# Kernel tuning notes

Hardware: AMD Instinct MI355X
Metric: run time of the kernel (lower is better)

## Reference

```python
import jax, jax.numpy as jnp
import numpy as np

NUM_HEADS = 16
HEAD_SIZE = 64
EMB = NUM_HEADS * HEAD_SIZE
B, S = 2, 2048


def setup_inputs() -> dict:
    key = jax.random.key(0)
    ks = jax.random.split(key, 8)
    return {
        "values": jax.random.normal(ks[0], (B, S, EMB), dtype=jnp.float32),
        "keys": jax.random.normal(ks[1], (B, S, EMB), dtype=jnp.float32),
        "queries": jax.random.normal(ks[2], (B, S, EMB), dtype=jnp.float32),
        "mask": jnp.ones((B, 1, 1, S), dtype=jnp.int32),
        "Wq": jax.random.normal(ks[3], (HEAD_SIZE, HEAD_SIZE), dtype=jnp.float32) / np.sqrt(HEAD_SIZE),
        "Wk": jax.random.normal(ks[4], (HEAD_SIZE, HEAD_SIZE), dtype=jnp.float32) / np.sqrt(HEAD_SIZE),
        "Wv": jax.random.normal(ks[5], (HEAD_SIZE, HEAD_SIZE), dtype=jnp.float32) / np.sqrt(HEAD_SIZE),
        "Wout": jax.random.normal(ks[6], (EMB, EMB), dtype=jnp.float32) / np.sqrt(EMB),
        "bout": jax.random.normal(ks[7], (EMB,), dtype=jnp.float32) * 0.01,
    }


def reference(values, keys, queries, mask, Wq, Wk, Wv, Wout, bout):
    n, q_len, E = queries.shape
    H, D = NUM_HEADS, HEAD_SIZE
    # split heads: [n, len, H, D]
    v = values.reshape(n, -1, H, D)
    k = keys.reshape(n, -1, H, D)
    q = queries.reshape(n, q_len, H, D)
    # per-head shared linears (torch Linear: x @ W.T), no bias
    v = jnp.einsum("nkhd,cd->nkhc", v, Wv)
    k = jnp.einsum("nkhd,cd->nkhc", k, Wk)
    q = jnp.einsum("nqhd,cd->nqhc", q, Wq)
    # scores: [n, H, q, k]
    energy = jnp.einsum("nqhd,nkhd->nhqk", q, k)
    energy = jnp.where(mask == 0, jnp.float32(-1e28), energy)
    # NOTE: source scales by sqrt(embedding_size), not head_size
    attn = jax.nn.softmax(energy / jnp.sqrt(jnp.float32(E)), axis=3)
    out = jnp.einsum("nhqk,nkhd->nqhd", attn, v).reshape(n, q_len, E)
    return out @ Wout.T + bout
```

## Files before the change

kernel.cpp:

```cpp
#include <hip/hip_runtime.h>
#include <hip/hip_bf16.h>


#define NHB 16
#define HS  64
#define EMB 1024
#define BB  2
#define SS  2048
#define NT  (SS / 64)

typedef __bf16 bf16_t;
typedef bf16_t bf16x8 __attribute__((ext_vector_type(8)));
typedef bf16_t bf16x4 __attribute__((ext_vector_type(4)));
typedef float  f32x4  __attribute__((ext_vector_type(4)));

__device__ __forceinline__ f32x4 mfma16(bf16x8 a, bf16x8 b, f32x4 c) {
    return __builtin_amdgcn_mfma_f32_16x16x32_bf16(a, b, c, 0, 0, 0);
}

__global__ __launch_bounds__(512) void proj_kernel(
    const float* __restrict__ queries, const float* __restrict__ keys,
    const float* __restrict__ values,
    const float* __restrict__ Wq, const float* __restrict__ Wk,
    const float* __restrict__ Wv,
    bf16_t* __restrict__ Qb, bf16_t* __restrict__ Kb, bf16_t* __restrict__ Vt)
{
    __shared__ bf16_t Ws[3][64][72];
    __shared__ bf16_t Xs[128][72];

    const int tid  = threadIdx.x;
    const int wave = tid >> 6, lane = tid & 63;
    const int q4 = lane >> 4, l16 = lane & 15;
    const int s0 = blockIdx.x * 128;
    const int h  = blockIdx.y, n = blockIdx.z;

    #pragma unroll
    for (int i = 0; i < 6; ++i) {
        int g = i * 512 + tid;
        int mW = g >> 10;
        int idx4 = g & 1023;
        const float* wp = (mW == 0) ? Wq : (mW == 1) ? Wk : Wv;
        float4 v = ((const float4*)wp)[idx4];
        int r = idx4 >> 4, c = (idx4 & 15) * 4;
        Ws[mW][r][c+0] = (bf16_t)v.x; Ws[mW][r][c+1] = (bf16_t)v.y;
        Ws[mW][r][c+2] = (bf16_t)v.z; Ws[mW][r][c+3] = (bf16_t)v.w;
    }

    const size_t headBase = (size_t)(n * NHB + h) * SS * HS;

    float4 gx[4];
    auto loadX = [&](const float* xp) {
        #pragma unroll
        for (int i = 0; i < 4; ++i) {
            int idx4 = i * 512 + tid;
            int r = idx4 >> 4, c = (idx4 & 15) * 4;
            gx[i] = *(const float4*)&xp[((size_t)(n * SS + s0 + r)) * EMB + h * HS + c];
        }
    };
    loadX(queries);

    for (int p = 0; p < 3; ++p) {
        __syncthreads();
        #pragma unroll
        for (int i = 0; i < 4; ++i) {
            int idx4 = i * 512 + tid;
            int r = idx4 >> 4, c = (idx4 & 15) * 4;
            Xs[r][c+0] = (bf16_t)gx[i].x; Xs[r][c+1] = (bf16_t)gx[i].y;
            Xs[r][c+2] = (bf16_t)gx[i].z; Xs[r][c+3] = (bf16_t)gx[i].w;
        }
        if (p == 0) loadX(keys);
        else if (p == 1) loadX(values);
        __syncthreads();

        bf16x8 xf[2], wf[4][2];
        #pragma unroll
        for (int kk = 0; kk < 2; ++kk)
            xf[kk] = *(const bf16x8*)&Xs[wave * 16 + l16][kk * 32 + q4 * 8];
        #pragma unroll
        for (int ct = 0; ct < 4; ++ct)
            #pragma unroll
            for (int kk = 0; kk < 2; ++kk)
                wf[ct][kk] = *(const bf16x8*)&Ws[p][ct * 16 + l16][kk * 32 + q4 * 8];

        if (p < 2) {
            bf16_t* dst = (p == 0) ? Qb : Kb;
            const float sc = (p == 0) ? 0.03125f : 1.0f;
            #pragma unroll
            for (int ct = 0; ct < 4; ++ct) {
                f32x4 acc = {};
                acc = mfma16(wf[ct][0], xf[0], acc);
                acc = mfma16(wf[ct][1], xf[1], acc);
                bf16x4 pk;
                #pragma unroll
                for (int i = 0; i < 4; ++i) pk[i] = (bf16_t)(acc[i] * sc);
                *(bf16x4*)&dst[headBase + (size_t)(s0 + wave * 16 + l16) * HS
                               + ct * 16 + q4 * 4] = pk;
            }
        } else {
            #pragma unroll
            for (int ct = 0; ct < 4; ++ct) {
                f32x4 acc = {};
                acc = mfma16(xf[0], wf[ct][0], acc);
                acc = mfma16(xf[1], wf[ct][1], acc);
                bf16x4 pk;
                #pragma unroll
                for (int i = 0; i < 4; ++i) pk[i] = (bf16_t)acc[i];
                *(bf16x4*)&Vt[headBase + (size_t)(ct * 16 + l16) * SS
                              + s0 + (wave >> 1) * 32 + q4 * 8 + (wave & 1) * 4] = pk;
            }
        }
    }
}

__global__ __launch_bounds__(512) void attn_kernel(
    const bf16_t* __restrict__ Qb, const bf16_t* __restrict__ Kb,
    const bf16_t* __restrict__ Vt, const int* __restrict__ mask,
    bf16_t* __restrict__ Og)
{
    __shared__ __align__(16) unsigned char smem[37376];
    auto Ks = (bf16_t(*)[64][72])(smem);
    auto Vs = (bf16_t(*)[64][72])(smem + 18432);
    auto Ms = (float(*)[64])(smem + 36864);
    float* fbuf = (float*)smem;
    float* lbuf = (float*)(smem + 32768);

    const int tid = threadIdx.x;
    const int w = tid >> 6, lane = tid & 63;
    const int q4 = lane >> 4, l16 = lane & 15;
    const int wq = w & 3, wk = w >> 2;
    const int qt = blockIdx.x, h = blockIdx.y, n = blockIdx.z;
    const size_t headBase = (size_t)(n * NHB + h) * SS * HS;
    const int* mrow = mask + n * SS;

    const int sr = tid >> 3, sc = (tid & 7) * 8;
    const bf16_t* kb_src = Kb + headBase + (size_t)sr * HS + sc;
    const bf16_t* vt_src = Vt + headBase + (size_t)sr * SS + sc;

    bf16x8 bq[2][2];
    #pragma unroll
    for (int st = 0; st < 2; ++st) {
        const bf16_t* qptr = Qb + headBase
            + (size_t)(qt * 128 + wq * 32 + st * 16 + l16) * HS;
        bq[st][0] = *(const bf16x8*)&qptr[q4 * 8];
        bq[st][1] = *(const bf16x8*)&qptr[32 + q4 * 8];
    }

    bf16x8 ones;
    #pragma unroll
    for (int i = 0; i < 8; ++i) ones[i] = (bf16_t)1.0f;

    f32x4 oaccT[2][4] = {};
    f32x4 lacc[2] = {};

    *(bf16x8*)&Ks[0][sr][sc] = *(const bf16x8*)kb_src;
    *(bf16x8*)&Vs[0][sr][sc] = *(const bf16x8*)vt_src;
    if (tid < 64) Ms[0][tid] = mrow[tid] ? 0.0f : -3e38f;
    __syncthreads();

    for (int kt = 0; kt < NT; ++kt) {
        const int cur = kt & 1;
        const bool has_next = (kt + 1) < NT;
        bf16x8 gk, gv; float gm = 0.f;
        if (has_next) {
            const int k0n = (kt + 1) * 64;
            gk = *(const bf16x8*)(kb_src + (size_t)k0n * HS);
            gv = *(const bf16x8*)(vt_src + k0n);
            if (tid < 64) gm = mrow[k0n + tid] ? 0.0f : -3e38f;
        }

        f32x4 sacc[2][2];
        #pragma unroll
        for (int c2 = 0; c2 < 2; ++c2) {
            const int ct = wk * 2 + c2;
            float4 bias = *(const float4*)&Ms[cur][ct * 16 + q4 * 4];
            f32x4 b4 = {bias.x, bias.y, bias.z, bias.w};
            sacc[0][c2] = b4; sacc[1][c2] = b4;
            bf16x8 ak0 = *(const bf16x8*)&Ks[cur][ct * 16 + l16][q4 * 8];
            bf16x8 ak1 = *(const bf16x8*)&Ks[cur][ct * 16 + l16][32 + q4 * 8];
            #pragma unroll
            for (int st = 0; st < 2; ++st) {
                sacc[st][c2] = mfma16(ak0, bq[st][0], sacc[st][c2]);
                sacc[st][c2] = mfma16(ak1, bq[st][1], sacc[st][c2]);
            }
        }

        bf16x4 pv[2][2];
        #pragma unroll
        for (int c2 = 0; c2 < 2; ++c2)
            #pragma unroll
            for (int st = 0; st < 2; ++st) {
                bf16x4 pk;
                #pragma unroll
                for (int j = 0; j < 4; ++j)
                    pk[j] = (bf16_t)__expf(sacc[st][c2][j]);
                pv[st][c2] = pk;
            }

        bf16x8 pa[2];
        #pragma unroll
        for (int st = 0; st < 2; ++st)
            pa[st] = __builtin_shufflevector(pv[st][0], pv[st][1],
                                             0, 1, 2, 3, 4, 5, 6, 7);
        #pragma unroll
        for (int dt = 0; dt < 4; ++dt) {
            bf16x8 av = *(const bf16x8*)&Vs[cur][dt * 16 + l16][wk * 32 + q4 * 8];
            oaccT[0][dt] = mfma16(av, pa[0], oaccT[0][dt]);
            oaccT[1][dt] = mfma16(av, pa[1], oaccT[1][dt]);
        }
        lacc[0] = mfma16(ones, pa[0], lacc[0]);
        lacc[1] = mfma16(ones, pa[1], lacc[1]);

        if (has_next) {
            const int nxt = 1 - cur;
            *(bf16x8*)&Ks[nxt][sr][sc] = gk;
            *(bf16x8*)&Vs[nxt][sr][sc] = gv;
            if (tid < 64) Ms[nxt][tid] = gm;
        }
        __syncthreads();
    }

    float ls[2] = {lacc[0][0], lacc[1][0]};

    if (w >= 4) {
        const int lanecol = wq * 64 + lane;
        #pragma unroll
        for (int st = 0; st < 2; ++st) {
            #pragma unroll
            for (int dt = 0; dt < 4; ++dt)
                #pragma unroll
                for (int j = 0; j < 4; ++j)
                    fbuf[(st * 16 + dt * 4 + j) * 256 + lanecol] = oaccT[st][dt][j];
            lbuf[st * 256 + lanecol] = ls[st];
        }
    }
    __syncthreads();
    if (w < 4) {
        const int lanecol = wq * 64 + lane;
        #pragma unroll
        for (int st = 0; st < 2; ++st) {
            #pragma unroll
            for (int dt = 0; dt < 4; ++dt)
                #pragma unroll
                for (int j = 0; j < 4; ++j)
                    oaccT[st][dt][j] += fbuf[(st * 16 + dt * 4 + j) * 256 + lanecol];
            ls[st] += lbuf[st * 256 + lanecol];
        }
        #pragma unroll
        for (int st = 0; st < 2; ++st) {
            const float inv = 1.f / ls[st];
            const int qrow = qt * 128 + wq * 32 + st * 16 + l16;
            bf16_t* obase = Og + ((size_t)(n * SS + qrow)) * EMB + h * HS;
            #pragma unroll
            for (int dt = 0; dt < 4; ++dt) {
                bf16x4 ov;
                #pragma unroll
                for (int j = 0; j < 4; ++j) ov[j] = (bf16_t)(oaccT[st][dt][j] * inv);
                *(bf16x4*)&obase[dt * 16 + q4 * 4] = ov;
            }
        }
    }
}

__global__ __launch_bounds__(512) void outproj_kernel(
    const bf16_t* __restrict__ Og, const float* __restrict__ Wout,
    const float* __restrict__ bout, float* __restrict__ out)
{
    __shared__ bf16_t As[2][128][72];
    __shared__ bf16_t Bs[2][64][72];
    const int tid = threadIdx.x;
    const int w = tid >> 6, lane = tid & 63;
    const int q4 = lane >> 4, l16 = lane & 15;
    const int wr = w >> 1, wc = w & 1;
    const int t0 = blockIdx.x * 128, c0 = blockIdx.y * 64;

    const int sr0 = tid >> 3, sc0 = (tid & 7) * 8;
    const int sr1 = sr0 + 64;
    const bf16_t* a0 = Og + (size_t)(t0 + sr0) * EMB + sc0;
    const bf16_t* a1 = Og + (size_t)(t0 + sr1) * EMB + sc0;
    const float*  b0 = Wout + (size_t)(c0 + sr0) * EMB + sc0;

    auto cvt8 = [](float4 x, float4 y) {
        bf16x8 r;
        r[0] = (bf16_t)x.x; r[1] = (bf16_t)x.y; r[2] = (bf16_t)x.z; r[3] = (bf16_t)x.w;
        r[4] = (bf16_t)y.x; r[5] = (bf16_t)y.y; r[6] = (bf16_t)y.z; r[7] = (bf16_t)y.w;
        return r;
    };

    f32x4 acc[2][2] = {};

    *(bf16x8*)&As[0][sr0][sc0] = *(const bf16x8*)a0;
    *(bf16x8*)&As[0][sr1][sc0] = *(const bf16x8*)a1;
    *(bf16x8*)&Bs[0][sr0][sc0] = cvt8(*(const float4*)b0, *(const float4*)(b0 + 4));
    __syncthreads();

    const int NE = EMB / 64;
    for (int et = 0; et < NE; ++et) {
        const int cur = et & 1;
        const bool has_next = (et + 1) < NE;
        bf16x8 ga0, ga1; float4 gb0, gb1;
        if (has_next) {
            const int e0 = (et + 1) * 64;
            ga0 = *(const bf16x8*)(a0 + e0); ga1 = *(const bf16x8*)(a1 + e0);
            gb0 = *(const float4*)(b0 + e0); gb1 = *(const float4*)(b0 + e0 + 4);
        }

        bf16x8 af[2][2], bfr[2][2];
        #pragma unroll
        for (int st = 0; st < 2; ++st)
            #pragma unroll
            for (int kk = 0; kk < 2; ++kk)
                af[st][kk] = *(const bf16x8*)&As[cur][wr * 32 + st * 16 + l16][kk * 32 + q4 * 8];
        #pragma unroll
        for (int ct = 0; ct < 2; ++ct)
            #pragma unroll
            for (int kk = 0; kk < 2; ++kk)
                bfr[ct][kk] = *(const bf16x8*)&Bs[cur][wc * 32 + ct * 16 + l16][kk * 32 + q4 * 8];
        #pragma unroll
        for (int st = 0; st < 2; ++st)
            #pragma unroll
            for (int ct = 0; ct < 2; ++ct) {
                acc[st][ct] = mfma16(af[st][0], bfr[ct][0], acc[st][ct]);
                acc[st][ct] = mfma16(af[st][1], bfr[ct][1], acc[st][ct]);
            }

        if (has_next) {
            const int nxt = 1 - cur;
            *(bf16x8*)&As[nxt][sr0][sc0] = ga0;
            *(bf16x8*)&As[nxt][sr1][sc0] = ga1;
            *(bf16x8*)&Bs[nxt][sr0][sc0] = cvt8(gb0, gb1);
        }
        __syncthreads();
    }

    #pragma unroll
    for (int ct = 0; ct < 2; ++ct) {
        const int c = c0 + wc * 32 + ct * 16 + l16;
        const float bias = bout[c];
        #pragma unroll
        for (int st = 0; st < 2; ++st)
            #pragma unroll
            for (int i = 0; i < 4; ++i)
                out[(size_t)(t0 + wr * 32 + st * 16 + q4 * 4 + i) * EMB + c]
                    = acc[st][ct][i] + bias;
    }
}

extern "C" void kernel_launch(void* const* d_in, const int* in_sizes, int n_in,
                              void* d_out, int out_size, void* d_ws, size_t ws_size,
                              hipStream_t stream)
{
    const float* values  = (const float*)d_in[0];
    const float* keys    = (const float*)d_in[1];
    const float* queries = (const float*)d_in[2];
    const int*   mask    = (const int*)d_in[3];
    const float* Wq      = (const float*)d_in[4];
    const float* Wk      = (const float*)d_in[5];
    const float* Wv      = (const float*)d_in[6];
    const float* Wout    = (const float*)d_in[7];
    const float* bout    = (const float*)d_in[8];
    float* out = (float*)d_out;

    const size_t M8 = 8ull * 1024 * 1024;
    bf16_t* Qb = (bf16_t*)d_ws;
    bf16_t* Kb = (bf16_t*)((char*)d_ws + 1 * M8);
    bf16_t* Vt = (bf16_t*)((char*)d_ws + 2 * M8);
    bf16_t* Og = (bf16_t*)((char*)d_ws + 3 * M8);

    proj_kernel<<<dim3(SS / 128, NHB, BB), 512, 0, stream>>>(
        queries, keys, values, Wq, Wk, Wv, Qb, Kb, Vt);
    attn_kernel<<<dim3(SS / 128, NHB, BB), 512, 0, stream>>>(
        Qb, Kb, Vt, mask, Og);
    outproj_kernel<<<dim3((BB * SS) / 128, EMB / 64), 512, 0, stream>>>(
        Og, Wout, bout, out);
}
```

Before: 171.2 us.

## Fuse three kernels into one cooperative persistent kernel with grid syncs

Merges the projection, attention and output-projection kernels into a single cooperative kernel of 512 blocks that separates the stages with grid-wide barriers, falling back to three launches if the cooperative launch fails. Block indices are flattened and shared memory becomes one raw buffer sized for the largest stage. This targets launch gaps between the kernels. It also widens the Q/K stores to 16-byte vectors by changing the projection output packing. The risks are grid-sync cost, shared memory sized for the largest stage lowering occupancy in every stage, and the requirement that all 512 blocks be co-resident.

After: 320.6 us. 87.3% more time.

```diff
diff --git a/kernel.cpp b/kernel.cpp
--- a/kernel.cpp
+++ b/kernel.cpp
@@ -1,5 +1,8 @@
 #include <hip/hip_runtime.h>
 #include <hip/hip_bf16.h>
+#include <hip/hip_cooperative_groups.h>
+
+namespace cg = cooperative_groups;
 
 
 #define NHB 16
@@ -18,21 +21,22 @@
     return __builtin_amdgcn_mfma_f32_16x16x32_bf16(a, b, c, 0, 0, 0);
 }
 
-__global__ __launch_bounds__(512) void proj_kernel(
+__device__ __forceinline__ void proj_body(
+    unsigned char* smem_raw, int bid,
     const float* __restrict__ queries, const float* __restrict__ keys,
     const float* __restrict__ values,
     const float* __restrict__ Wq, const float* __restrict__ Wk,
     const float* __restrict__ Wv,
     bf16_t* __restrict__ Qb, bf16_t* __restrict__ Kb, bf16_t* __restrict__ Vt)
 {
-    __shared__ bf16_t Ws[3][64][72];
-    __shared__ bf16_t Xs[128][72];
+    auto Ws = (bf16_t(*)[64][72])(smem_raw);
+    auto Xs = (bf16_t(*)[72])(smem_raw + 27648);
 
     const int tid  = threadIdx.x;
     const int wave = tid >> 6, lane = tid & 63;
     const int q4 = lane >> 4, l16 = lane & 15;
-    const int s0 = blockIdx.x * 128;
-    const int h  = blockIdx.y, n = blockIdx.z;
+    const int s0 = (bid & 15) * 128;
+    const int h  = (bid >> 4) & 15, n = bid >> 8;
 
     #pragma unroll
     for (int i = 0; i < 6; ++i) {
@@ -85,17 +89,23 @@
         if (p < 2) {
             bf16_t* dst = (p == 0) ? Qb : Kb;
             const float sc = (p == 0) ? 0.03125f : 1.0f;
+            bf16x8 lo, hi;
             #pragma unroll
             for (int ct = 0; ct < 4; ++ct) {
                 f32x4 acc = {};
                 acc = mfma16(wf[ct][0], xf[0], acc);
                 acc = mfma16(wf[ct][1], xf[1], acc);
-                bf16x4 pk;
-                #pragma unroll
-                for (int i = 0; i < 4; ++i) pk[i] = (bf16_t)(acc[i] * sc);
-                *(bf16x4*)&dst[headBase + (size_t)(s0 + wave * 16 + l16) * HS
-                               + ct * 16 + q4 * 4] = pk;
-            }
+                #pragma unroll
+                for (int i = 0; i < 4; ++i) {
+                    bf16_t v = (bf16_t)(acc[i] * sc);
+                    if (ct < 2) lo[ct * 4 + i] = v;
+                    else        hi[(ct - 2) * 4 + i] = v;
+                }
+            }
+            bf16_t* rp = dst + headBase
+                + (size_t)(s0 + wave * 16 + l16) * HS + q4 * 16;
+            *(bf16x8*)rp = lo;
+            *(bf16x8*)(rp + 8) = hi;
         } else {
             #pragma unroll
             for (int ct = 0; ct < 4; ++ct) {
@@ -112,23 +122,23 @@
     }
 }
 
-__global__ __launch_bounds__(512) void attn_kernel(
+__device__ __forceinline__ void attn_body(
+    unsigned char* smem_raw, int bid,
     const bf16_t* __restrict__ Qb, const bf16_t* __restrict__ Kb,
     const bf16_t* __restrict__ Vt, const int* __restrict__ mask,
     bf16_t* __restrict__ Og)
 {
-    __shared__ __align__(16) unsigned char smem[37376];
-    auto Ks = (bf16_t(*)[64][72])(smem);
-    auto Vs = (bf16_t(*)[64][72])(smem + 18432);
-    auto Ms = (float(*)[64])(smem + 36864);
-    float* fbuf = (float*)smem;
-    float* lbuf = (float*)(smem + 32768);
+    auto Ks = (bf16_t(*)[64][72])(smem_raw);
+    auto Vs = (bf16_t(*)[64][72])(smem_raw + 18432);
+    auto Ms = (float(*)[64])(smem_raw + 36864);
+    float* fbuf = (float*)smem_raw;
+    float* lbuf = (float*)(smem_raw + 32768);
 
     const int tid = threadIdx.x;
     const int w = tid >> 6, lane = tid & 63;
     const int q4 = lane >> 4, l16 = lane & 15;
     const int wq = w & 3, wk = w >> 2;
-    const int qt = blockIdx.x, h = blockIdx.y, n = blockIdx.z;
+    const int qt = bid & 15, h = (bid >> 4) & 15, n = bid >> 8;
     const size_t headBase = (size_t)(n * NHB + h) * SS * HS;
     const int* mrow = mask + n * SS;
 
@@ -261,17 +271,19 @@
     }
 }
 
-__global__ __launch_bounds__(512) void outproj_kernel(
+__device__ __forceinline__ void outproj_body(
+    unsigned char* smem_raw, int bid,
     const bf16_t* __restrict__ Og, const float* __restrict__ Wout,
     const float* __restrict__ bout, float* __restrict__ out)
 {
-    __shared__ bf16_t As[2][128][72];
-    __shared__ bf16_t Bs[2][64][72];
+    auto As = (bf16_t(*)[128][72])(smem_raw);
+    auto Bs = (bf16_t(*)[64][72])(smem_raw + 36864);
+
     const int tid = threadIdx.x;
     const int w = tid >> 6, lane = tid & 63;
     const int q4 = lane >> 4, l16 = lane & 15;
     const int wr = w >> 1, wc = w & 1;
-    const int t0 = blockIdx.x * 128, c0 = blockIdx.y * 64;
+    const int t0 = (bid & 31) * 128, c0 = (bid >> 5) * 64;
 
     const int sr0 = tid >> 3, sc0 = (tid & 7) * 8;
     const int sr1 = sr0 + 64;
@@ -343,6 +355,47 @@
                 out[(size_t)(t0 + wr * 32 + st * 16 + q4 * 4 + i) * EMB + c]
                     = acc[st][ct][i] + bias;
     }
+}
+
+__global__ __launch_bounds__(512) void fused_kernel(
+    const float* values, const float* keys, const float* queries,
+    const int* mask, const float* Wq, const float* Wk, const float* Wv,
+    const float* Wout, const float* bout, float* out,
+    bf16_t* Qb, bf16_t* Kb, bf16_t* Vt, bf16_t* Og)
+{
+    __shared__ __align__(16) unsigned char smem[55296];
+    cg::grid_group grid = cg::this_grid();
+    const int bid = blockIdx.x;
+
+    proj_body(smem, bid, queries, keys, values, Wq, Wk, Wv, Qb, Kb, Vt);
+    grid.sync();
+    attn_body(smem, bid, Qb, Kb, Vt, mask, Og);
+    grid.sync();
+    outproj_body(smem, bid, Og, Wout, bout, out);
+}
+
+__global__ __launch_bounds__(512) void proj_k(
+    const float* queries, const float* keys, const float* values,
+    const float* Wq, const float* Wk, const float* Wv,
+    bf16_t* Qb, bf16_t* Kb, bf16_t* Vt)
+{
+    __shared__ __align__(16) unsigned char smem[46080];
+    proj_body(smem, blockIdx.x, queries, keys, values, Wq, Wk, Wv, Qb, Kb, Vt);
+}
+
+__global__ __launch_bounds__(512) void attn_k(
+    const bf16_t* Qb, const bf16_t* Kb, const bf16_t* Vt,
+    const int* mask, bf16_t* Og)
+{
+    __shared__ __align__(16) unsigned char smem[37376];
+    attn_body(smem, blockIdx.x, Qb, Kb, Vt, mask, Og);
+}
+
+__global__ __launch_bounds__(512) void outproj_k(
+    const bf16_t* Og, const float* Wout, const float* bout, float* out)
+{
+    __shared__ __align__(16) unsigned char smem[55296];
+    outproj_body(smem, blockIdx.x, Og, Wout, bout, out);
 }
 
 extern "C" void kernel_launch(void* const* d_in, const int* in_sizes, int n_in,
@@ -366,10 +419,18 @@
     bf16_t* Vt = (bf16_t*)((char*)d_ws + 2 * M8);
     bf16_t* Og = (bf16_t*)((char*)d_ws + 3 * M8);
 
-    proj_kernel<<<dim3(SS / 128, NHB, BB), 512, 0, stream>>>(
-        queries, keys, values, Wq, Wk, Wv, Qb, Kb, Vt);
-    attn_kernel<<<dim3(SS / 128, NHB, BB), 512, 0, stream>>>(
-        Qb, Kb, Vt, mask, Og);
-    outproj_kernel<<<dim3((BB * SS) / 128, EMB / 64), 512, 0, stream>>>(
-        Og, Wout, bout, out);
-}
+    void* args[] = {
+        (void*)&values, (void*)&keys, (void*)&queries, (void*)&mask,
+        (void*)&Wq, (void*)&Wk, (void*)&Wv, (void*)&Wout, (void*)&bout,
+        (void*)&out, (void*)&Qb, (void*)&Kb, (void*)&Vt, (void*)&Og,
+    };
+    hipError_t err = hipLaunchCooperativeKernel(
+        (const void*)fused_kernel, dim3(512), dim3(512), args, 0, stream);
+    if (err != hipSuccess) {
+        (void)hipGetLastError();
+        proj_k<<<dim3(512), 512, 0, stream>>>(
+            queries, keys, values, Wq, Wk, Wv, Qb, Kb, Vt);
+        attn_k<<<dim3(512), 512, 0, stream>>>(Qb, Kb, Vt, mask, Og);
+        outproj_k<<<dim3(512), 512, 0, stream>>>(Og, Wout, bout, out);
+    }
+}
```

## Halve attention query tile to 64 rows with 256 threads; vectorize Q/K stores

Applied to the files above, without the earlier changes.

The attention kernel now handles 64 query rows per block with 4 waves instead of 128 rows with 8 waves. That doubles the grid to 1024 blocks, giving more blocks per CU and better load balance. Each thread now loads two K/V rows per tile to fill the shared-memory stage, and the split-K reduction buffers are resized to match. Separately, the projection kernel packs Q/K outputs into two 16-byte stores per lane, which permutes the head dimension identically for Q and K so their dot products are unchanged. The cost is that K/V tiles are read from global/L2 twice as often across the grid.

New measurement: 192.2 us. +12.3%, slower.

```diff
diff --git a/kernel.cpp b/kernel.cpp
--- a/kernel.cpp
+++ b/kernel.cpp
@@ -85,17 +85,23 @@
         if (p < 2) {
             bf16_t* dst = (p == 0) ? Qb : Kb;
             const float sc = (p == 0) ? 0.03125f : 1.0f;
+            bf16x8 lo, hi;
             #pragma unroll
             for (int ct = 0; ct < 4; ++ct) {
                 f32x4 acc = {};
                 acc = mfma16(wf[ct][0], xf[0], acc);
                 acc = mfma16(wf[ct][1], xf[1], acc);
-                bf16x4 pk;
-                #pragma unroll
-                for (int i = 0; i < 4; ++i) pk[i] = (bf16_t)(acc[i] * sc);
-                *(bf16x4*)&dst[headBase + (size_t)(s0 + wave * 16 + l16) * HS
-                               + ct * 16 + q4 * 4] = pk;
-            }
+                #pragma unroll
+                for (int i = 0; i < 4; ++i) {
+                    bf16_t v = (bf16_t)(acc[i] * sc);
+                    if (ct < 2) lo[ct * 4 + i] = v;
+                    else        hi[(ct - 2) * 4 + i] = v;
+                }
+            }
+            bf16_t* rp = dst + headBase
+                + (size_t)(s0 + wave * 16 + l16) * HS + q4 * 16;
+            *(bf16x8*)rp = lo;
+            *(bf16x8*)(rp + 8) = hi;
         } else {
             #pragma unroll
             for (int ct = 0; ct < 4; ++ct) {
@@ -112,7 +118,7 @@
     }
 }
 
-__global__ __launch_bounds__(512) void attn_kernel(
+__global__ __launch_bounds__(256) void attn_kernel(
     const bf16_t* __restrict__ Qb, const bf16_t* __restrict__ Kb,
     const bf16_t* __restrict__ Vt, const int* __restrict__ mask,
     bf16_t* __restrict__ Og)
@@ -122,25 +128,28 @@
     auto Vs = (bf16_t(*)[64][72])(smem + 18432);
     auto Ms = (float(*)[64])(smem + 36864);
     float* fbuf = (float*)smem;
-    float* lbuf = (float*)(smem + 32768);
+    float* lbuf = (float*)(smem + 16384);
 
     const int tid = threadIdx.x;
     const int w = tid >> 6, lane = tid & 63;
     const int q4 = lane >> 4, l16 = lane & 15;
-    const int wq = w & 3, wk = w >> 2;
+    const int wq = w & 1, wk = w >> 1;
     const int qt = blockIdx.x, h = blockIdx.y, n = blockIdx.z;
     const size_t headBase = (size_t)(n * NHB + h) * SS * HS;
     const int* mrow = mask + n * SS;
 
-    const int sr = tid >> 3, sc = (tid & 7) * 8;
-    const bf16_t* kb_src = Kb + headBase + (size_t)sr * HS + sc;
-    const bf16_t* vt_src = Vt + headBase + (size_t)sr * SS + sc;
+    const int sr0 = tid >> 3, sc0 = (tid & 7) * 8;
+    const int sr1 = sr0 + 32;
+    const bf16_t* kb0 = Kb + headBase + (size_t)sr0 * HS + sc0;
+    const bf16_t* kb1 = Kb + headBase + (size_t)sr1 * HS + sc0;
+    const bf16_t* vt0 = Vt + headBase + (size_t)sr0 * SS + sc0;
+    const bf16_t* vt1 = Vt + headBase + (size_t)sr1 * SS + sc0;
 
     bf16x8 bq[2][2];
     #pragma unroll
     for (int st = 0; st < 2; ++st) {
         const bf16_t* qptr = Qb + headBase
-            + (size_t)(qt * 128 + wq * 32 + st * 16 + l16) * HS;
+            + (size_t)(qt * 64 + wq * 32 + st * 16 + l16) * HS;
         bq[st][0] = *(const bf16x8*)&qptr[q4 * 8];
         bq[st][1] = *(const bf16x8*)&qptr[32 + q4 * 8];
     }
@@ -152,19 +161,23 @@
     f32x4 oaccT[2][4] = {};
     f32x4 lacc[2] = {};
 
-    *(bf16x8*)&Ks[0][sr][sc] = *(const bf16x8*)kb_src;
-    *(bf16x8*)&Vs[0][sr][sc] = *(const bf16x8*)vt_src;
+    *(bf16x8*)&Ks[0][sr0][sc0] = *(const bf16x8*)kb0;
+    *(bf16x8*)&Ks[0][sr1][sc0] = *(const bf16x8*)kb1;
+    *(bf16x8*)&Vs[0][sr0][sc0] = *(const bf16x8*)vt0;
+    *(bf16x8*)&Vs[0][sr1][sc0] = *(const bf16x8*)vt1;
     if (tid < 64) Ms[0][tid] = mrow[tid] ? 0.0f : -3e38f;
     __syncthreads();
 
     for (int kt = 0; kt < NT; ++kt) {
         const int cur = kt & 1;
         const bool has_next = (kt + 1) < NT;
-        bf16x8 gk, gv; float gm = 0.f;
+        bf16x8 gk0, gk1, gv0, gv1; float gm = 0.f;
         if (has_next) {
             const int k0n = (kt + 1) * 64;
-            gk = *(const bf16x8*)(kb_src + (size_t)k0n * HS);
-            gv = *(const bf16x8*)(vt_src + k0n);
+            gk0 = *(const bf16x8*)(kb0 + (size_t)k0n * HS);
+            gk1 = *(const bf16x8*)(kb1 + (size_t)k0n * HS);
+            gv0 = *(const bf16x8*)(vt0 + k0n);
+            gv1 = *(const bf16x8*)(vt1 + k0n);
             if (tid < 64) gm = mrow[k0n + tid] ? 0.0f : -3e38f;
         }
 
@@ -212,8 +225,10 @@
 
         if (has_next) {
             const int nxt = 1 - cur;
-            *(bf16x8*)&Ks[nxt][sr][sc] = gk;
-            *(bf16x8*)&Vs[nxt][sr][sc] = gv;
+            *(bf16x8*)&Ks[nxt][sr0][sc0] = gk0;
+            *(bf16x8*)&Ks[nxt][sr1][sc0] = gk1;
+            *(bf16x8*)&Vs[nxt][sr0][sc0] = gv0;
+            *(bf16x8*)&Vs[nxt][sr1][sc0] = gv1;
             if (tid < 64) Ms[nxt][tid] = gm;
         }
         __syncthreads();
@@ -221,7 +236,7 @@
 
     float ls[2] = {lacc[0][0], lacc[1][0]};
 
-    if (w >= 4) {
+    if (w >= 2) {
         const int lanecol = wq * 64 + lane;
         #pragma unroll
         for (int st = 0; st < 2; ++st) {
@@ -229,12 +244,12 @@
             for (int dt = 0; dt < 4; ++dt)
                 #pragma unroll
                 for (int j = 0; j < 4; ++j)
-                    fbuf[(st * 16 + dt * 4 + j) * 256 + lanecol] = oaccT[st][dt][j];
-            lbuf[st * 256 + lanecol] = ls[st];
+                    fbuf[(st * 16 + dt * 4 + j) * 128 + lanecol] = oaccT[st][dt][j];
+            lbuf[st * 128 + lanecol] = ls[st];
         }
     }
     __syncthreads();
-    if (w < 4) {
+    if (w < 2) {
         const int lanecol = wq * 64 + lane;
         #pragma unroll
         for (int st = 0; st < 2; ++st) {
@@ -242,13 +257,13 @@
             for (int dt = 0; dt < 4; ++dt)
                 #pragma unroll
                 for (int j = 0; j < 4; ++j)
-                    oaccT[st][dt][j] += fbuf[(st * 16 + dt * 4 + j) * 256 + lanecol];
-            ls[st] += lbuf[st * 256 + lanecol];
+                    oaccT[st][dt][j] += fbuf[(st * 16 + dt * 4 + j) * 128 + lanecol];
+            ls[st] += lbuf[st * 128 + lanecol];
         }
         #pragma unroll
         for (int st = 0; st < 2; ++st) {
             const float inv = 1.f / ls[st];
-            const int qrow = qt * 128 + wq * 32 + st * 16 + l16;
+            const int qrow = qt * 64 + wq * 32 + st * 16 + l16;
             bf16_t* obase = Og + ((size_t)(n * SS + qrow)) * EMB + h * HS;
             #pragma unroll
             for (int dt = 0; dt < 4; ++dt) {
@@ -368,7 +383,7 @@
 
     proj_kernel<<<dim3(SS / 128, NHB, BB), 512, 0, stream>>>(
         queries, keys, values, Wq, Wk, Wv, Qb, Kb, Vt);
-    attn_kernel<<<dim3(SS / 128, NHB, BB), 512, 0, stream>>>(
+    attn_kernel<<<dim3(SS / 64, NHB, BB), 256, 0, stream>>>(
         Qb, Kb, Vt, mask, Og);
     outproj_kernel<<<dim3((BB * SS) / 128, EMB / 64), 512, 0, stream>>>(
         Og, Wout, bout, out);
```
